# Kernel tuning notes

Hardware: AMD Instinct MI355X
Metric: run time of the kernel (lower is better)

The kernel has to match this reference:

```python
import jax, jax.numpy as jnp
import numpy as np

N, C, H, W = 8, 256, 52, 52
N_WIN, NUM_HEADS, TOPK = 7, 1, 4
RS = (H // N_WIN, W // N_WIN)  # region size (7, 7)
SCALE = C ** -0.5


def _avg_pool_ceil(t):
    # F.avg_pool2d(kernel=RS, stride=RS, ceil_mode=True, count_include_pad=False)
    B, Ch, h_in, w_in = t.shape
    h = -(-h_in // RS[0]); w = -(-w_in // RS[1])
    tp = jnp.pad(t, ((0, 0), (0, 0), (0, h * RS[0] - h_in), (0, w * RS[1] - w_in)))
    s = tp.reshape(B, Ch, h, RS[0], w, RS[1]).sum(axis=(3, 5))
    rc = np.minimum(RS[0], h_in - np.arange(h) * RS[0]).astype(np.float32)
    cc = np.minimum(RS[1], w_in - np.arange(w) * RS[1]).astype(np.float32)
    return s / (rc[:, None] * cc[None, :])


def _nearest_up(t):
    # F.interpolate(mode='nearest', scale_factor=RS) for integer scales == repeat
    return jnp.repeat(jnp.repeat(t, RS[0], axis=2), RS[1], axis=3)


def _grid2seq(t):
    # BCHW -> (B, nhead, nregion, reg_area, head_dim)
    B, Ch, Hp, Wp = t.shape
    rh, rw = Hp // RS[0], Wp // RS[1]
    hd = Ch // NUM_HEADS
    t = t.reshape(B, NUM_HEADS, hd, rh, RS[0], rw, RS[1]).transpose(0, 1, 3, 5, 4, 6, 2)
    return t.reshape(B, NUM_HEADS, rh * rw, RS[0] * RS[1], hd), rh, rw


def _forward(x, y, q_w, q_b, k_w, k_b):
    q = jnp.einsum('nchw,oc->nohw', x, q_w) + q_b[None, :, None, None]
    k = jnp.einsum('nchw,oc->nohw', y, k_w) + k_b[None, :, None, None]
    # routing path uses detached q, k
    q_r = _avg_pool_ceil(jax.lax.stop_gradient(q))  # (B, C, 8, 8)
    k_r = _avg_pool_ceil(jax.lax.stop_gradient(k))
    B, _, h, w = q_r.shape
    nreg = h * w
    a_r = jnp.einsum('nchw,ncyx->nhwyx', q_r, k_r).reshape(B, nreg, nreg)
    idx = jax.lax.top_k(a_r, TOPK)[1]                              # (B, nreg, topk)
    idx = jnp.broadcast_to(idx[:, None], (B, NUM_HEADS, nreg, TOPK))
    a_r = SCALE * a_r
    # coarse scores upsampled over key pixels, then over query pixels
    a1 = _nearest_up(a_r.reshape(B, nreg, h, w))                   # (B, nreg, Hp, Wp)
    Hp, Wp = a1.shape[2], a1.shape[3]
    a1 = _nearest_up(a1.transpose(0, 2, 3, 1).reshape(B, Hp * Wp, h, w))  # (B, Hp*Wp, Hp, Wp)
    reg_area = (Hp * Wp) // nreg
    a6 = a1.reshape(B, NUM_HEADS, nreg, reg_area // NUM_HEADS, nreg, reg_area)
    # fine attention on padded q, k
    pad_b = (RS[0] - H % RS[0]) % RS[0]
    pad_r = (RS[1] - W % RS[1]) % RS[1]
    qp = jnp.pad(q, ((0, 0), (0, 0), (0, pad_b), (0, pad_r)))
    kp = jnp.pad(k, ((0, 0), (0, 0), (0, pad_b), (0, pad_r)))
    q_seq, rh, rw = _grid2seq(qp)   # (B, nh, nreg, reg_area, hd)
    k_seq, _, _ = _grid2seq(kp)
    bI = jnp.arange(B)[:, None, None, None]
    mI = jnp.arange(NUM_HEADS)[None, :, None, None]
    key_g = k_seq[bI, mI, idx]      # gather top-k key regions: (B, nh, nreg, topk, reg_area, hd)
    attn = jnp.einsum('bmrqd,bmrtkd->bmrqtk', q_seq * SCALE, key_g)
    # torch.scatter along dim 4 with index repeated over the t' axis -> duplicate
    # writes to the same slot; serial torch scatter keeps the LAST write (t'=TOPK-1)
    vals = attn[:, :, :, :TOPK, TOPK - 1, :]  # (B, nh, nreg, topk, reg_area)
    rI = jnp.arange(nreg)[None, None, :, None]
    tI = jnp.arange(TOPK)[None, None, None, :]
    corr = a6.at[bI, mI, rI, tI, idx].set(vals)
    # _corr2grid: 10-dim view + 'bmhwpqyxcd->bmhpwqycxd'
    c10 = corr.reshape(B, NUM_HEADS, rh, rw, RS[0], RS[1], rh, rw, RS[0], RS[1])
    c10 = c10.transpose(0, 1, 2, 4, 3, 5, 6, 8, 7, 9)
    Hf, Wf = rh * RS[0], rw * RS[1]
    corr = c10.reshape(B, NUM_HEADS, Hf, Wf, Hf, Wf)
    corr = corr[:, :, :Hf - pad_b, :Wf - pad_r, :Hf - pad_b, :Wf - pad_r]
    return corr.transpose(0, 2, 3, 1, 4, 5)  # (B, H, W, nhead, H, W)


def setup_inputs():
    ks = jax.random.split(jax.random.key(0), 6)
    return {
        'x': jax.random.normal(ks[0], (N, C, H, W), jnp.float32),
        'y': jax.random.normal(ks[1], (N, C, H, W), jnp.float32),
        'q_w': jax.random.normal(ks[2], (C, C), jnp.float32) * (C ** -0.5),
        'q_b': jax.random.normal(ks[3], (C,), jnp.float32) * 0.02,
        'k_w': jax.random.normal(ks[4], (C, C), jnp.float32) * (C ** -0.5),
        'k_b': jax.random.normal(ks[5], (C,), jnp.float32) * 0.02,
    }


def reference(x, y, q_w, q_b, k_w, k_b):
    return _forward(x, y, q_w, q_b, k_w, k_b)
```

## Files before the change

kernel.cpp:

```cpp
#include <hip/hip_runtime.h>

#define NB 8
#define C 256
#define HW 52
#define P (HW*HW)
#define NTOPK 4
#define SCALE 0.0625f

static __device__ __forceinline__ int d7(int v)  { return (v*9363) >> 16; }
static __device__ __forceinline__ int d56(int v) { return (v*18725) >> 20; }
static __device__ __forceinline__ int d13(int v) { return (v*10083) >> 17; }

#define OFF_YR  0
#define OFF_XGT 131072
#define OFF_XRT 655360
#define OFF_M   786432
#define OFF_U   851968
#define OFF_V2  852224
#define OFF_C0  852480
#define OFF_YT  852496

__global__ __launch_bounds__(256) void k1_pool_prep_tr(
    const float* __restrict__ x, const float* __restrict__ y,
    const float* __restrict__ qw, const float* __restrict__ qb,
    const float* __restrict__ kw, const float* __restrict__ kb,
    float* __restrict__ scr)
{
    __shared__ float sm[4*P];
    const int tid = threadIdx.x;
    const int bx = blockIdx.x;

    float* yr  = scr + OFF_YR;
    float* xgT = scr + OFF_XGT;
    float* xrT = scr + OFF_XRT;
    float* M   = scr + OFF_M;
    float* u   = scr + OFF_U;
    float* v2  = scr + OFF_V2;
    float* c0p = scr + OFF_C0;
    float* yT  = scr + OFF_YT;

    if (bx >= 1089) {
        const int tb = bx - 1089;
        const int b = tb / 172;
        const int rem = tb - b*172;
        const int ct = rem / 43;
        const int pt = rem - ct*43;
        const int c0 = ct*64, pos0 = pt*64;
        float* tile = sm;
        const float* ysrc = y + ((size_t)(b*256 + c0))*P;
        #pragma unroll
        for (int p = 0; p < 4; p++) {
            const int cr = p*16 + (tid>>4);
            const int f4 = tid&15;
            const int pos = pos0 + f4*4;
            if (pos < P) {
                const float4 v = *(const float4*)(ysrc + (size_t)cr*P + pos);
                float* d = tile + cr*65 + f4*4;
                d[0]=v.x; d[1]=v.y; d[2]=v.z; d[3]=v.w;
            }
        }
        __syncthreads();
        #pragma unroll
        for (int p = 0; p < 4; p++) {
            const int pj = p*16 + (tid>>4);
            const int c4 = tid&15;
            const int pos = pos0 + pj;
            if (pos < P) {
                float4 v;
                v.x = tile[(c4*4+0)*65 + pj];
                v.y = tile[(c4*4+1)*65 + pj];
                v.z = tile[(c4*4+2)*65 + pj];
                v.w = tile[(c4*4+3)*65 + pj];
                *(float4*)(yT + ((size_t)(b*P + pos))*256 + c0 + c4*4) = v;
            }
        }
        return;
    }

    if (bx >= 1024) {
        const int pb = bx - 1024;
        if (pb == 64) {
            float ua = 0.f, va = 0.f;
            for (int e = 0; e < 256; e++) {
                ua += qb[e] * kw[e*256 + tid];
                va += kb[e] * qw[e*256 + tid];
            }
            u[tid] = ua; v2[tid] = va;
            if (tid == 0) {
                float c = 0.f;
                for (int e = 0; e < 256; e++) c += qb[e]*kb[e];
                c0p[0] = c;
            }
            return;
        }
        const int cx0 = pb * 4;
        float (*wqs)[4] = (float(*)[4])sm;
        *(float4*)&wqs[tid][0] = *(const float4*)(qw + tid*256 + cx0);
        __syncthreads();
        float a0=0.f, a1=0.f, a2=0.f, a3=0.f;
        #pragma unroll 4
        for (int o = 0; o < 256; o++) {
            const float wk = kw[o*256 + tid];
            const float4 wq = *(const float4*)&wqs[o][0];
            a0 += wq.x*wk; a1 += wq.y*wk; a2 += wq.z*wk; a3 += wq.w*wk;
        }
        M[(cx0+0)*256 + tid] = a0;
        M[(cx0+1)*256 + tid] = a1;
        M[(cx0+2)*256 + tid] = a2;
        M[(cx0+3)*256 + tid] = a3;
        return;
    }

    const int w = tid >> 6, lane = tid & 63;
    const int pl = bx*4 + w;
    const int proj = pl >> 11;
    const int bcid = pl & 2047;
    const int bb = bcid >> 8, cc = bcid & 255;
    const float* src = (proj ? y : x) + (size_t)bcid * P;
    float* plane = sm + w*P;
    {
        const float4* s4 = (const float4*)src;
        float4* p4 = (float4*)plane;
        for (int g = lane; g < 676; g += 64) p4[g] = s4[g];
    }
    __syncthreads();
    const int jh = lane >> 3, jw = lane & 7;
    const int y0 = jh*7, x0 = jw*7;
    const int ry = min(7, HW - y0), rx = min(7, HW - x0);
    float s = 0.f;
    for (int dy = 0; dy < ry; ++dy) {
        const float* row = plane + (y0 + dy)*HW + x0;
        for (int dx = 0; dx < rx; ++dx) s += row[dx];
    }
    const float pooled = s / (float)(ry*rx);
    if (proj) {
        yr[bcid*64 + lane] = pooled;
    } else {
        xrT[((size_t)(bb*64) + lane)*256 + cc] = pooled;
        const float* r0 = plane + y0*HW + x0;
        #pragma unroll
        for (int t = 0; t < 4; t++) {
            const float v = (x0 + t < HW) ? r0[t] : 0.f;
            xgT[((size_t)(bb*256) + lane*4 + t)*256 + cc] = v;
        }
    }
}

__global__ __launch_bounds__(256) void k2_topk_vals(
    const float* __restrict__ scr,
    float* __restrict__ arT, int* __restrict__ idxout, float* __restrict__ vals)
{
    const int b = blockIdx.y, r = blockIdx.x;
    const int tid = threadIdx.x, w = tid >> 6, lane = tid & 63;

    const float* yr  = scr + OFF_YR;
    const float* xgT = scr + OFF_XGT;
    const float* xrT = scr + OFF_XRT;
    const float* M   = scr + OFF_M;
    const float* u   = scr + OFF_U;
    const float* v2  = scr + OFF_V2;
    const float* c0p = scr + OFF_C0;
    const float* yT  = scr + OFF_YT;

    __shared__ float Gs[4][256];
    __shared__ float Grs[256];
    __shared__ float pdot[4][64];
    __shared__ float aux[12];
    __shared__ int gsh;
    __shared__ float Ys[49][260];

    const float* xrow0 = xgT + ((size_t)(b*256) + r*4)*256;
    const float* xrow4 = xrT + ((size_t)(b*64) + r)*256;
    {
        float a0=0.f, a1=0.f, a2=0.f, a3=0.f, a4=0.f;
        #pragma unroll 4
        for (int c = 0; c < 256; c++) {
            const float m = M[c*256 + tid];
            a0 += xrow0[c]       * m;
            a1 += xrow0[256 + c] * m;
            a2 += xrow0[512 + c] * m;
            a3 += xrow0[768 + c] * m;
            a4 += xrow4[c]       * m;
        }
        const float uo = u[tid];
        Gs[0][tid] = a0 + uo;
        Gs[1][tid] = a1 + uo;
        Gs[2][tid] = a2 + uo;
        Gs[3][tid] = a3 + uo;
        Grs[tid]   = a4 + uo;
    }
    {
        const float* xh = xrow0 + w*256;
        float hacc = 0.f;
        #pragma unroll
        for (int j = 0; j < 4; j++) {
            const int c = lane + j*64;
            hacc += xh[c] * v2[c];
        }
        #pragma unroll
        for (int off = 32; off >= 1; off >>= 1) hacc += __shfl_xor(hacc, off);
        if (lane == 0) aux[w] = hacc + c0p[0];

        float cacc = xrow4[w*64 + lane] * v2[w*64 + lane];
        #pragma unroll
        for (int off = 32; off >= 1; off >>= 1) cacc += __shfl_xor(cacc, off);
        if (lane == 0) aux[4 + w] = cacc;
    }
    __syncthreads();

    {
        const float* yrB = yr + b*C*64;
        float d = 0.f;
        #pragma unroll 8
        for (int cc = 0; cc < 64; cc++) {
            const int c = w*64 + cc;
            d += Grs[c] * yrB[c*64 + lane];
        }
        pdot[w][lane] = d;
    }
    __syncthreads();

    if (w == 0) {
        const float ci = aux[4] + aux[5] + aux[6] + aux[7] + c0p[0];
        const float dot = pdot[0][lane] + pdot[1][lane] + pdot[2][lane]
                        + pdot[3][lane] + ci;
        arT[(b*64 + lane)*64 + r] = dot * SCALE;
        float v = dot;
        const int my = lane;
        #pragma unroll
        for (int t = 0; t < NTOPK; t++) {
            float bv = v; int bi = my;
            #pragma unroll
            for (int off = 32; off >= 1; off >>= 1) {
                const float ov = __shfl_xor(bv, off);
                const int   oi = __shfl_xor(bi, off);
                if (ov > bv || (ov == bv && oi < bi)) { bv = ov; bi = oi; }
            }
            if (lane == 0) {
                idxout[(b*64 + r)*NTOPK + t] = bi;
                if (t == NTOPK-1) gsh = bi;
            }
            if (my == bi) v = -3.0e38f;
        }
    }
    __syncthreads();

    const int g = gsh;
    const int gy = g >> 3, gx = g & 7;
    for (int i = tid; i < 49*64; i += 256) {
        const int k2 = i >> 6, f4 = i & 63;
        const int dy = d7(k2), dx = k2 - dy*7;
        const int kY = gy*7 + dy, kX = gx*7 + dx;
        float4 v = make_float4(0.f, 0.f, 0.f, 0.f);
        if (kY < HW && kX < HW)
            v = *(const float4*)(yT + ((size_t)(b*P + kY*HW + kX))*256 + f4*4);
        *(float4*)&Ys[k2][f4*4] = v;
    }
    __syncthreads();

    if (tid < NTOPK*49) {
        const int t = tid / 49, k2 = tid - (tid/49)*49;
        const int qX = (r & 7)*7 + t;
        const int dy = d7(k2), dx = k2 - dy*7;
        const int kY = gy*7 + dy, kX = gx*7 + dx;
        float res = 0.f;
        if (qX < HW && kY < HW && kX < HW) {
            const float4* Gp = (const float4*)&Gs[t][0];
            const float4* Yp = (const float4*)&Ys[k2][0];
            float dot = 0.f;
            #pragma unroll 8
            for (int cc = 0; cc < 64; cc++) {
                const float4 a = Gp[cc], yy = Yp[cc];
                dot += a.x*yy.x + a.y*yy.y + a.z*yy.z + a.w*yy.w;
            }
            res = SCALE * (dot + aux[t]);
        }
        vals[((b*64 + r)*NTOPK + t)*49 + k2] = res;
    }
}

__global__ __launch_bounds__(256) void fill_kernel(
    const float* __restrict__ arT, const float* __restrict__ vals,
    const int* __restrict__ idx, float* __restrict__ out)
{
    const int b = blockIdx.y;
    const int yx = blockIdx.x;
    const int Y1 = yx / HW, X1 = yx % HW;
    const int r1 = (Y1/7)*8 + X1/7;
    const int q1 = (Y1%7)*7 + X1%7;
    const int p2 = r1*49 + q1;
    const int yy = p2/56, xx = p2 - 56*yy;
    const int regB = (yy/7)*8 + xx/7;

    __shared__ float acol[64];
    __shared__ float vrow[49];
    const int tid = threadIdx.x;
    if (tid < 64) acol[tid] = arT[(b*64 + regB)*64 + tid];
    int ovr = -1;
    if (q1 < NTOPK) {
        ovr = idx[(b*64 + r1)*NTOPK + q1];
        if (tid < 49) vrow[tid] = vals[((b*64 + r1)*NTOPK + q1)*49 + tid];
    }
    __syncthreads();

    float* plane = out + (size_t)(b*P + yx) * P;
    for (int u = tid; u < 676; u += 256) {
        const int Y2 = d13(u);
        const int g4 = u - Y2*13;
        const int X2b = g4*4;
        const int ry2 = d7(Y2);
        const int my2 = Y2 - ry2*7;
        float res[4];
        #pragma unroll
        for (int j = 0; j < 4; j++) {
            const int X2 = X2b + j;
            const int rx2 = d7(X2);
            const int mx2 = X2 - rx2*7;
            const int r2 = ry2*8 + rx2;
            const int k2 = my2*7 + mx2;
            const int P1 = r2*49 + k2;
            const int Yp = d56(P1);
            const int Xp = P1 - Yp*56;
            const int regA = d7(Yp)*8 + d7(Xp);
            float v = acol[regA];
            if (r2 == ovr) v = vrow[k2];
            res[j] = v;
        }
        float4 o; o.x = res[0]; o.y = res[1]; o.z = res[2]; o.w = res[3];
        *(float4*)(plane + Y2*HW + X2b) = o;
    }
}

extern "C" void kernel_launch(void* const* d_in, const int* in_sizes, int n_in,
                              void* d_out, int out_size, void* d_ws, size_t ws_size,
                              hipStream_t stream)
{
    const float* x  = (const float*)d_in[0];
    const float* y  = (const float*)d_in[1];
    const float* qw = (const float*)d_in[2];
    const float* qb = (const float*)d_in[3];
    const float* kw = (const float*)d_in[4];
    const float* kb = (const float*)d_in[5];
    float* out = (float*)d_out;

    float* scr = out;

    float* ws  = (float*)d_ws;
    float* arT = ws;
    float* vls = arT + 32768;
    int*   idx = (int*)(vls + 100352);

    k1_pool_prep_tr<<<2465, 256, 0, stream>>>(x, y, qw, qb, kw, kb, scr);
    k2_topk_vals<<<dim3(64, 8), 256, 0, stream>>>(scr, arT, idx, vls);
    fill_kernel<<<dim3(P, 8), 256, 0, stream>>>(arT, vls, idx, out);
}
```

Baseline: 116.7 us.

## Split projection GEMM into a tiled shared-memory kernel before top-k

Moves the per-block G = X·M products out of the top-k kernel into a dedicated tiled GEMM kernel with 64x64 shared-memory tiles and 4x4 register blocking. Pooled and gathered x are now stored channel-major with coalesced float4 writes instead of scattered transposed stores. The top-k kernel then just loads the precomputed G rows. The final output fill uses nontemporal stores. This adds a kernel launch and an extra scratch round trip, and the h-term reads in the top-k kernel become strided.

```diff
diff --git a/kernel.cpp b/kernel.cpp
--- a/kernel.cpp
+++ b/kernel.cpp
@@ -7,18 +7,22 @@
 #define NTOPK 4
 #define SCALE 0.0625f
 
+typedef float nt_f32x4 __attribute__((ext_vector_type(4)));
+
 static __device__ __forceinline__ int d7(int v)  { return (v*9363) >> 16; }
 static __device__ __forceinline__ int d56(int v) { return (v*18725) >> 20; }
 static __device__ __forceinline__ int d13(int v) { return (v*10083) >> 17; }
 
-#define OFF_YR  0
-#define OFF_XGT 131072
-#define OFF_XRT 655360
-#define OFF_M   786432
-#define OFF_U   851968
-#define OFF_V2  852224
-#define OFF_C0  852480
-#define OFF_YT  852496
+#define OFF_XR  0
+#define OFF_YR  131072
+#define OFF_XG  262144
+#define OFF_G   786432
+#define OFF_GR  1310720
+#define OFF_M   1441792
+#define OFF_U   1507328
+#define OFF_V2  1507584
+#define OFF_C0  1507840
+#define OFF_YT  1507856
 
 __global__ __launch_bounds__(256) void k1_pool_prep_tr(
     const float* __restrict__ x, const float* __restrict__ y,
@@ -30,9 +34,9 @@
     const int tid = threadIdx.x;
     const int bx = blockIdx.x;
 
+    float* xr  = scr + OFF_XR;
     float* yr  = scr + OFF_YR;
-    float* xgT = scr + OFF_XGT;
-    float* xrT = scr + OFF_XRT;
+    float* xg  = scr + OFF_XG;
     float* M   = scr + OFF_M;
     float* u   = scr + OFF_U;
     float* v2  = scr + OFF_V2;
@@ -115,7 +119,6 @@
     const int pl = bx*4 + w;
     const int proj = pl >> 11;
     const int bcid = pl & 2047;
-    const int bb = bcid >> 8, cc = bcid & 255;
     const float* src = (proj ? y : x) + (size_t)bcid * P;
     float* plane = sm + w*P;
     {
@@ -136,28 +139,92 @@
     if (proj) {
         yr[bcid*64 + lane] = pooled;
     } else {
-        xrT[((size_t)(bb*64) + lane)*256 + cc] = pooled;
+        xr[bcid*64 + lane] = pooled;
         const float* r0 = plane + y0*HW + x0;
-        #pragma unroll
-        for (int t = 0; t < 4; t++) {
-            const float v = (x0 + t < HW) ? r0[t] : 0.f;
-            xgT[((size_t)(bb*256) + lane*4 + t)*256 + cc] = v;
-        }
+        float4 g4;
+        g4.x = r0[0]; g4.y = r0[1]; g4.z = r0[2];
+        g4.w = (x0 + 3 < HW) ? r0[3] : 0.f;
+        *(float4*)&xg[bcid*256 + lane*4] = g4;
     }
 }
 
-__global__ __launch_bounds__(256) void k2_topk_vals(
+__global__ __launch_bounds__(256) void k2_gemms(float* __restrict__ scr)
+{
+    const float* xr = scr + OFF_XR;
+    const float* xg = scr + OFF_XG;
+    float* G  = scr + OFF_G;
+    float* Gr = scr + OFF_GR;
+    const float* M  = scr + OFF_M;
+    const float* uu = scr + OFF_U;
+
+    __shared__ float As[32][64];
+    __shared__ float Bs[32][64];
+    const int tid = threadIdx.x;
+    const int tx = tid & 15, ty = tid >> 4;
+
+    const int un = blockIdx.x;
+    const int b = un / 20;
+    const int rem = un - b*20;
+    const int pt = rem >> 2, ot = rem & 3;
+    const int o0 = ot*64;
+
+    float acc[4][4];
+    #pragma unroll
+    for (int i = 0; i < 4; i++)
+        #pragma unroll
+        for (int j = 0; j < 4; j++) acc[i][j] = 0.f;
+
+    const int lkr = tid >> 3;
+    const int ljc = (tid & 7) * 8;
+    const float* Asrc; int astr;
+    if (pt < 4) { Asrc = xg + (size_t)b*C*256 + pt*64; astr = 256; }
+    else        { Asrc = xr + (size_t)b*C*64;          astr = 64;  }
+
+    for (int k0 = 0; k0 < 256; k0 += 32) {
+        const float4 a0 = *(const float4*)(Asrc + (size_t)(k0 + lkr)*astr + ljc);
+        const float4 a1 = *(const float4*)(Asrc + (size_t)(k0 + lkr)*astr + ljc + 4);
+        const float4 b0 = *(const float4*)(M + (k0 + lkr)*256 + o0 + ljc);
+        const float4 b1 = *(const float4*)(M + (k0 + lkr)*256 + o0 + ljc + 4);
+        __syncthreads();
+        *(float4*)&As[lkr][ljc] = a0; *(float4*)&As[lkr][ljc+4] = a1;
+        *(float4*)&Bs[lkr][ljc] = b0; *(float4*)&Bs[lkr][ljc+4] = b1;
+        __syncthreads();
+        #pragma unroll
+        for (int kk = 0; kk < 32; kk++) {
+            const float4 a = *(const float4*)&As[kk][ty*4];
+            const float4 bb = *(const float4*)&Bs[kk][tx*4];
+            const float av[4] = {a.x, a.y, a.z, a.w};
+            const float bv[4] = {bb.x, bb.y, bb.z, bb.w};
+            #pragma unroll
+            for (int i = 0; i < 4; i++)
+                #pragma unroll
+                for (int j = 0; j < 4; j++) acc[i][j] += av[i]*bv[j];
+        }
+    }
+    const float4 u4 = *(const float4*)(uu + o0 + tx*4);
+    float* base = (pt < 4) ? (G + ((size_t)b*256 + pt*64)*256)
+                           : (Gr + (size_t)b*64*256);
+    #pragma unroll
+    for (int i = 0; i < 4; i++) {
+        float4 ov;
+        ov.x = acc[i][0]+u4.x; ov.y = acc[i][1]+u4.y;
+        ov.z = acc[i][2]+u4.z; ov.w = acc[i][3]+u4.w;
+        *(float4*)(base + (ty*4 + i)*256 + o0 + tx*4) = ov;
+    }
+}
+
+__global__ __launch_bounds__(256) void k3_topk_vals(
     const float* __restrict__ scr,
     float* __restrict__ arT, int* __restrict__ idxout, float* __restrict__ vals)
 {
     const int b = blockIdx.y, r = blockIdx.x;
     const int tid = threadIdx.x, w = tid >> 6, lane = tid & 63;
 
+    const float* xr  = scr + OFF_XR;
     const float* yr  = scr + OFF_YR;
-    const float* xgT = scr + OFF_XGT;
-    const float* xrT = scr + OFF_XRT;
-    const float* M   = scr + OFF_M;
-    const float* u   = scr + OFF_U;
+    const float* xg  = scr + OFF_XG;
+    const float* G   = scr + OFF_G;
+    const float* Gr  = scr + OFF_GR;
     const float* v2  = scr + OFF_V2;
     const float* c0p = scr + OFF_C0;
     const float* yT  = scr + OFF_YT;
@@ -169,39 +236,24 @@
     __shared__ int gsh;
     __shared__ float Ys[49][260];
 
-    const float* xrow0 = xgT + ((size_t)(b*256) + r*4)*256;
-    const float* xrow4 = xrT + ((size_t)(b*64) + r)*256;
+    *(float4*)&Gs[w][lane*4] =
+        *(const float4*)(G + ((size_t)(b*256 + r*4 + w))*256 + lane*4);
+    if (tid < 64)
+        *(float4*)&Grs[tid*4] = *(const float4*)(Gr + ((size_t)(b*64 + r))*256 + tid*4);
     {
-        float a0=0.f, a1=0.f, a2=0.f, a3=0.f, a4=0.f;
-        #pragma unroll 4
-        for (int c = 0; c < 256; c++) {
-            const float m = M[c*256 + tid];
-            a0 += xrow0[c]       * m;
-            a1 += xrow0[256 + c] * m;
-            a2 += xrow0[512 + c] * m;
-            a3 += xrow0[768 + c] * m;
-            a4 += xrow4[c]       * m;
-        }
-        const float uo = u[tid];
-        Gs[0][tid] = a0 + uo;
-        Gs[1][tid] = a1 + uo;
-        Gs[2][tid] = a2 + uo;
-        Gs[3][tid] = a3 + uo;
-        Grs[tid]   = a4 + uo;
-    }
-    {
-        const float* xh = xrow0 + w*256;
+        const int pos = r*4 + w;
         float hacc = 0.f;
         #pragma unroll
         for (int j = 0; j < 4; j++) {
             const int c = lane + j*64;
-            hacc += xh[c] * v2[c];
+            hacc += xg[((size_t)(b*256 + c))*256 + pos] * v2[c];
         }
         #pragma unroll
         for (int off = 32; off >= 1; off >>= 1) hacc += __shfl_xor(hacc, off);
         if (lane == 0) aux[w] = hacc + c0p[0];
 
-        float cacc = xrow4[w*64 + lane] * v2[w*64 + lane];
+        const int c = w*64 + lane;
+        float cacc = xr[(size_t)(b*256 + c)*64 + r] * v2[c];
         #pragma unroll
         for (int off = 32; off >= 1; off >>= 1) cacc += __shfl_xor(cacc, off);
         if (lane == 0) aux[4 + w] = cacc;
@@ -326,8 +378,9 @@
             if (r2 == ovr) v = vrow[k2];
             res[j] = v;
         }
-        float4 o; o.x = res[0]; o.y = res[1]; o.z = res[2]; o.w = res[3];
-        *(float4*)(plane + Y2*HW + X2b) = o;
+        nt_f32x4 o;
+        o.x = res[0]; o.y = res[1]; o.z = res[2]; o.w = res[3];
+        __builtin_nontemporal_store(o, (nt_f32x4*)(plane + Y2*HW + X2b));
     }
 }
 
@@ -351,6 +404,7 @@
     int*   idx = (int*)(vls + 100352);
 
     k1_pool_prep_tr<<<2465, 256, 0, stream>>>(x, y, qw, qb, kw, kb, scr);
-    k2_topk_vals<<<dim3(64, 8), 256, 0, stream>>>(scr, arT, idx, vls);
+    k2_gemms<<<160, 256, 0, stream>>>(scr);
+    k3_topk_vals<<<dim3(64, 8), 256, 0, stream>>>(scr, arT, idx, vls);
     fill_kernel<<<dim3(P, 8), 256, 0, stream>>>(arT, vls, idx, out);
 }
```

New measurement: 106.5 us. 8.7% less time.

## Split projection GEMM into separate wide kernel and coalesce transposed pooled writes

Applied to the files above, without the earlier changes.

Moves the per-region G = x·M projection out of the 512-block topk kernel into a new 640-block kernel that also hosts the y transpose, so the GEMM runs across many more workgroups. The pooling kernel now stages its pooled and gathered values in shared memory and writes them as float4 across four channels, replacing scattered scalar stores. The fill kernel uses nontemporal stores for the large output. This costs an extra launch and an extra round trip of G through global memory.

```diff
diff --git a/kernel.cpp b/kernel.cpp
--- a/kernel.cpp
+++ b/kernel.cpp
@@ -7,6 +7,8 @@
 #define NTOPK 4
 #define SCALE 0.0625f
 
+typedef float nt_f32x4 __attribute__((ext_vector_type(4)));
+
 static __device__ __forceinline__ int d7(int v)  { return (v*9363) >> 16; }
 static __device__ __forceinline__ int d56(int v) { return (v*18725) >> 20; }
 static __device__ __forceinline__ int d13(int v) { return (v*10083) >> 17; }
@@ -14,19 +16,23 @@
 #define OFF_YR  0
 #define OFF_XGT 131072
 #define OFF_XRT 655360
-#define OFF_M   786432
-#define OFF_U   851968
-#define OFF_V2  852224
-#define OFF_C0  852480
-#define OFF_YT  852496
-
-__global__ __launch_bounds__(256) void k1_pool_prep_tr(
+#define OFF_G   786432
+#define OFF_GR  1310720
+#define OFF_M   1441792
+#define OFF_U   1507328
+#define OFF_V2  1507584
+#define OFF_C0  1507840
+#define OFF_YT  1507856
+
+__global__ __launch_bounds__(256) void ka_pool_prep(
     const float* __restrict__ x, const float* __restrict__ y,
     const float* __restrict__ qw, const float* __restrict__ qb,
     const float* __restrict__ kw, const float* __restrict__ kb,
     float* __restrict__ scr)
 {
     __shared__ float sm[4*P];
+    __shared__ float gbuf[4][256];
+    __shared__ float pbuf[4][64];
     const int tid = threadIdx.x;
     const int bx = blockIdx.x;
 
@@ -37,45 +43,6 @@
     float* u   = scr + OFF_U;
     float* v2  = scr + OFF_V2;
     float* c0p = scr + OFF_C0;
-    float* yT  = scr + OFF_YT;
-
-    if (bx >= 1089) {
-        const int tb = bx - 1089;
-        const int b = tb / 172;
-        const int rem = tb - b*172;
-        const int ct = rem / 43;
-        const int pt = rem - ct*43;
-        const int c0 = ct*64, pos0 = pt*64;
-        float* tile = sm;
-        const float* ysrc = y + ((size_t)(b*256 + c0))*P;
-        #pragma unroll
-        for (int p = 0; p < 4; p++) {
-            const int cr = p*16 + (tid>>4);
-            const int f4 = tid&15;
-            const int pos = pos0 + f4*4;
-            if (pos < P) {
-                const float4 v = *(const float4*)(ysrc + (size_t)cr*P + pos);
-                float* d = tile + cr*65 + f4*4;
-                d[0]=v.x; d[1]=v.y; d[2]=v.z; d[3]=v.w;
-            }
-        }
-        __syncthreads();
-        #pragma unroll
-        for (int p = 0; p < 4; p++) {
-            const int pj = p*16 + (tid>>4);
-            const int c4 = tid&15;
-            const int pos = pos0 + pj;
-            if (pos < P) {
-                float4 v;
-                v.x = tile[(c4*4+0)*65 + pj];
-                v.y = tile[(c4*4+1)*65 + pj];
-                v.z = tile[(c4*4+2)*65 + pj];
-                v.w = tile[(c4*4+3)*65 + pj];
-                *(float4*)(yT + ((size_t)(b*P + pos))*256 + c0 + c4*4) = v;
-            }
-        }
-        return;
-    }
 
     if (bx >= 1024) {
         const int pb = bx - 1024;
@@ -115,7 +82,6 @@
     const int pl = bx*4 + w;
     const int proj = pl >> 11;
     const int bcid = pl & 2047;
-    const int bb = bcid >> 8, cc = bcid & 255;
     const float* src = (proj ? y : x) + (size_t)bcid * P;
     float* plane = sm + w*P;
     {
@@ -136,17 +102,115 @@
     if (proj) {
         yr[bcid*64 + lane] = pooled;
     } else {
-        xrT[((size_t)(bb*64) + lane)*256 + cc] = pooled;
+        pbuf[w][lane] = pooled;
         const float* r0 = plane + y0*HW + x0;
-        #pragma unroll
-        for (int t = 0; t < 4; t++) {
-            const float v = (x0 + t < HW) ? r0[t] : 0.f;
-            xgT[((size_t)(bb*256) + lane*4 + t)*256 + cc] = v;
+        gbuf[w][lane*4+0] = r0[0];
+        gbuf[w][lane*4+1] = r0[1];
+        gbuf[w][lane*4+2] = r0[2];
+        gbuf[w][lane*4+3] = (x0 + 3 < HW) ? r0[3] : 0.f;
+        __syncthreads();
+        const int pl0 = bx*4;
+        const int b  = (pl0 & 2047) >> 8;
+        const int c0 = pl0 & 255;
+        {
+            const int pos = tid;
+            float4 v;
+            v.x = gbuf[0][pos]; v.y = gbuf[1][pos];
+            v.z = gbuf[2][pos]; v.w = gbuf[3][pos];
+            *(float4*)(xgT + ((size_t)(b*256 + pos))*256 + c0) = v;
+        }
+        if (tid < 64) {
+            float4 v;
+            v.x = pbuf[0][tid]; v.y = pbuf[1][tid];
+            v.z = pbuf[2][tid]; v.w = pbuf[3][tid];
+            *(float4*)(xrT + ((size_t)(b*64 + tid))*256 + c0) = v;
         }
     }
 }
 
-__global__ __launch_bounds__(256) void k2_topk_vals(
+__global__ __launch_bounds__(256) void kb_gemm_tr(
+    const float* __restrict__ y, float* __restrict__ scr)
+{
+    __shared__ float sm[4160];
+    const int tid = threadIdx.x;
+    const int bx = blockIdx.x;
+
+    const float* xgT = scr + OFF_XGT;
+    const float* xrT = scr + OFF_XRT;
+    const float* M   = scr + OFF_M;
+    const float* uu  = scr + OFF_U;
+    float* G  = scr + OFF_G;
+    float* Gr = scr + OFF_GR;
+    float* yT = scr + OFF_YT;
+
+    if (bx < 640) {
+        const int b = bx / 80;
+        const int pg = bx - b*80;
+        float (*xs)[256] = (float(*)[256])sm;
+        #pragma unroll
+        for (int j = 0; j < 4; j++) {
+            const int R = pg*4 + j;
+            const float* src = (R < 256) ? (xgT + ((size_t)(b*256 + R))*256)
+                                         : (xrT + ((size_t)(b*64 + (R-256)))*256);
+            xs[j][tid] = src[tid];
+        }
+        __syncthreads();
+        float a0=0.f, a1=0.f, a2=0.f, a3=0.f;
+        #pragma unroll 8
+        for (int c = 0; c < 256; c++) {
+            const float m = M[c*256 + tid];
+            a0 += xs[0][c]*m; a1 += xs[1][c]*m;
+            a2 += xs[2][c]*m; a3 += xs[3][c]*m;
+        }
+        const float uo = uu[tid];
+        const float acc[4] = {a0+uo, a1+uo, a2+uo, a3+uo};
+        #pragma unroll
+        for (int j = 0; j < 4; j++) {
+            const int R = pg*4 + j;
+            float* dst = (R < 256) ? (G + ((size_t)(b*256 + R))*256)
+                                   : (Gr + ((size_t)(b*64 + (R-256)))*256);
+            dst[tid] = acc[j];
+        }
+        return;
+    }
+
+    const int tb = bx - 640;
+    const int b = tb / 172;
+    const int rem = tb - b*172;
+    const int ct = rem / 43;
+    const int pt = rem - ct*43;
+    const int c0 = ct*64, pos0 = pt*64;
+    float* tile = sm;
+    const float* ysrc = y + ((size_t)(b*256 + c0))*P;
+    #pragma unroll
+    for (int p = 0; p < 4; p++) {
+        const int cr = p*16 + (tid>>4);
+        const int f4 = tid&15;
+        const int pos = pos0 + f4*4;
+        if (pos < P) {
+            const float4 v = *(const float4*)(ysrc + (size_t)cr*P + pos);
+            float* d = tile + cr*65 + f4*4;
+            d[0]=v.x; d[1]=v.y; d[2]=v.z; d[3]=v.w;
+        }
+    }
+    __syncthreads();
+    #pragma unroll
+    for (int p = 0; p < 4; p++) {
+        const int pj = p*16 + (tid>>4);
+        const int c4 = tid&15;
+        const int pos = pos0 + pj;
+        if (pos < P) {
+            float4 v;
+            v.x = tile[(c4*4+0)*65 + pj];
+            v.y = tile[(c4*4+1)*65 + pj];
+            v.z = tile[(c4*4+2)*65 + pj];
+            v.w = tile[(c4*4+3)*65 + pj];
+            *(float4*)(yT + ((size_t)(b*P + pos))*256 + c0 + c4*4) = v;
+        }
+    }
+}
+
+__global__ __launch_bounds__(256) void kc_topk_vals(
     const float* __restrict__ scr,
     float* __restrict__ arT, int* __restrict__ idxout, float* __restrict__ vals)
 {
@@ -156,8 +220,8 @@
     const float* yr  = scr + OFF_YR;
     const float* xgT = scr + OFF_XGT;
     const float* xrT = scr + OFF_XRT;
-    const float* M   = scr + OFF_M;
-    const float* u   = scr + OFF_U;
+    const float* G   = scr + OFF_G;
+    const float* Gr  = scr + OFF_GR;
     const float* v2  = scr + OFF_V2;
     const float* c0p = scr + OFF_C0;
     const float* yT  = scr + OFF_YT;
@@ -169,39 +233,25 @@
     __shared__ int gsh;
     __shared__ float Ys[49][260];
 
-    const float* xrow0 = xgT + ((size_t)(b*256) + r*4)*256;
-    const float* xrow4 = xrT + ((size_t)(b*64) + r)*256;
+    *(float4*)&Gs[w][lane*4] =
+        *(const float4*)(G + ((size_t)(b*256 + r*4 + w))*256 + lane*4);
+    if (tid < 64)
+        *(float4*)&Grs[tid*4] = *(const float4*)(Gr + ((size_t)(b*64 + r))*256 + tid*4);
     {
-        float a0=0.f, a1=0.f, a2=0.f, a3=0.f, a4=0.f;
-        #pragma unroll 4
-        for (int c = 0; c < 256; c++) {
-            const float m = M[c*256 + tid];
-            a0 += xrow0[c]       * m;
-            a1 += xrow0[256 + c] * m;
-            a2 += xrow0[512 + c] * m;
-            a3 += xrow0[768 + c] * m;
-            a4 += xrow4[c]       * m;
-        }
-        const float uo = u[tid];
-        Gs[0][tid] = a0 + uo;
-        Gs[1][tid] = a1 + uo;
-        Gs[2][tid] = a2 + uo;
-        Gs[3][tid] = a3 + uo;
-        Grs[tid]   = a4 + uo;
-    }
-    {
-        const float* xh = xrow0 + w*256;
+        const float* xrow = xgT + ((size_t)(b*256 + r*4 + w))*256;
         float hacc = 0.f;
         #pragma unroll
         for (int j = 0; j < 4; j++) {
             const int c = lane + j*64;
-            hacc += xh[c] * v2[c];
+            hacc += xrow[c] * v2[c];
         }
         #pragma unroll
         for (int off = 32; off >= 1; off >>= 1) hacc += __shfl_xor(hacc, off);
         if (lane == 0) aux[w] = hacc + c0p[0];
 
-        float cacc = xrow4[w*64 + lane] * v2[w*64 + lane];
+        const float* rrow = xrT + ((size_t)(b*64 + r))*256;
+        const int c = w*64 + lane;
+        float cacc = rrow[c] * v2[c];
         #pragma unroll
         for (int off = 32; off >= 1; off >>= 1) cacc += __shfl_xor(cacc, off);
         if (lane == 0) aux[4 + w] = cacc;
@@ -279,7 +329,7 @@
     }
 }
 
-__global__ __launch_bounds__(256) void fill_kernel(
+__global__ __launch_bounds__(256) void kd_fill(
     const float* __restrict__ arT, const float* __restrict__ vals,
     const int* __restrict__ idx, float* __restrict__ out)
 {
@@ -326,8 +376,9 @@
             if (r2 == ovr) v = vrow[k2];
             res[j] = v;
         }
-        float4 o; o.x = res[0]; o.y = res[1]; o.z = res[2]; o.w = res[3];
-        *(float4*)(plane + Y2*HW + X2b) = o;
+        nt_f32x4 o;
+        o.x = res[0]; o.y = res[1]; o.z = res[2]; o.w = res[3];
+        __builtin_nontemporal_store(o, (nt_f32x4*)(plane + Y2*HW + X2b));
     }
 }
 
@@ -350,7 +401,8 @@
     float* vls = arT + 32768;
     int*   idx = (int*)(vls + 100352);
 
-    k1_pool_prep_tr<<<2465, 256, 0, stream>>>(x, y, qw, qb, kw, kb, scr);
-    k2_topk_vals<<<dim3(64, 8), 256, 0, stream>>>(scr, arT, idx, vls);
-    fill_kernel<<<dim3(P, 8), 256, 0, stream>>>(arT, vls, idx, out);
+    ka_pool_prep<<<1089, 256, 0, stream>>>(x, y, qw, qb, kw, kb, scr);
+    kb_gemm_tr<<<2016, 256, 0, stream>>>(y, scr);
+    kc_topk_vals<<<dim3(64, 8), 256, 0, stream>>>(scr, arT, idx, vls);
+    kd_fill<<<dim3(P, 8), 256, 0, stream>>>(arT, vls, idx, out);
 }
```

After: 108.2 us. 1.08x faster.

## Coalesce transposed scratch writes, stage x rows in LDS, use nontemporal output stores

Applied to the files above, without the earlier changes.

The pooling kernel now gathers the four channel planes of a block into shared buffers and writes the transposed xgT/xrT rows as float4 stores, replacing strided scalar scatters. The routing kernel first loads its five x rows into shared memory and reads them from there in the M-product and dot-product loops, with a higher unroll. The fill kernel writes its large output with nontemporal stores to avoid polluting cache. The change adds a block-wide barrier on the x-projection path and one more shared-memory staging step. Kernels are also renamed.

```diff
diff --git a/kernel.cpp b/kernel.cpp
--- a/kernel.cpp
+++ b/kernel.cpp
@@ -6,6 +6,8 @@
 #define P (HW*HW)
 #define NTOPK 4
 #define SCALE 0.0625f
+
+typedef float nt_f32x4 __attribute__((ext_vector_type(4)));
 
 static __device__ __forceinline__ int d7(int v)  { return (v*9363) >> 16; }
 static __device__ __forceinline__ int d56(int v) { return (v*18725) >> 20; }
@@ -20,13 +22,15 @@
 #define OFF_C0  852480
 #define OFF_YT  852496
 
-__global__ __launch_bounds__(256) void k1_pool_prep_tr(
+__global__ __launch_bounds__(256) void ka_pool_prep_tr(
     const float* __restrict__ x, const float* __restrict__ y,
     const float* __restrict__ qw, const float* __restrict__ qb,
     const float* __restrict__ kw, const float* __restrict__ kb,
     float* __restrict__ scr)
 {
     __shared__ float sm[4*P];
+    __shared__ float gbuf[4][256];
+    __shared__ float pbuf[4][64];
     const int tid = threadIdx.x;
     const int bx = blockIdx.x;
 
@@ -115,7 +119,6 @@
     const int pl = bx*4 + w;
     const int proj = pl >> 11;
     const int bcid = pl & 2047;
-    const int bb = bcid >> 8, cc = bcid & 255;
     const float* src = (proj ? y : x) + (size_t)bcid * P;
     float* plane = sm + w*P;
     {
@@ -136,17 +139,33 @@
     if (proj) {
         yr[bcid*64 + lane] = pooled;
     } else {
-        xrT[((size_t)(bb*64) + lane)*256 + cc] = pooled;
+        pbuf[w][lane] = pooled;
         const float* r0 = plane + y0*HW + x0;
-        #pragma unroll
-        for (int t = 0; t < 4; t++) {
-            const float v = (x0 + t < HW) ? r0[t] : 0.f;
-            xgT[((size_t)(bb*256) + lane*4 + t)*256 + cc] = v;
+        gbuf[w][lane*4+0] = r0[0];
+        gbuf[w][lane*4+1] = r0[1];
+        gbuf[w][lane*4+2] = r0[2];
+        gbuf[w][lane*4+3] = (x0 + 3 < HW) ? r0[3] : 0.f;
+        __syncthreads();
+        const int pl0 = bx*4;
+        const int b  = (pl0 & 2047) >> 8;
+        const int c0 = pl0 & 255;
+        {
+            const int pos = tid;
+            float4 v;
+            v.x = gbuf[0][pos]; v.y = gbuf[1][pos];
+            v.z = gbuf[2][pos]; v.w = gbuf[3][pos];
+            *(float4*)(xgT + ((size_t)(b*256 + pos))*256 + c0) = v;
+        }
+        if (tid < 64) {
+            float4 v;
+            v.x = pbuf[0][tid]; v.y = pbuf[1][tid];
+            v.z = pbuf[2][tid]; v.w = pbuf[3][tid];
+            *(float4*)(xrT + ((size_t)(b*64 + tid))*256 + c0) = v;
         }
     }
 }
 
-__global__ __launch_bounds__(256) void k2_topk_vals(
+__global__ __launch_bounds__(256) void kb_topk_vals(
     const float* __restrict__ scr,
     float* __restrict__ arT, int* __restrict__ idxout, float* __restrict__ vals)
 {
@@ -157,11 +176,12 @@
     const float* xgT = scr + OFF_XGT;
     const float* xrT = scr + OFF_XRT;
     const float* M   = scr + OFF_M;
-    const float* u   = scr + OFF_U;
+    const float* uu  = scr + OFF_U;
     const float* v2  = scr + OFF_V2;
     const float* c0p = scr + OFF_C0;
     const float* yT  = scr + OFF_YT;
 
+    __shared__ float xs[5][256];
     __shared__ float Gs[4][256];
     __shared__ float Grs[256];
     __shared__ float pdot[4][64];
@@ -169,20 +189,22 @@
     __shared__ int gsh;
     __shared__ float Ys[49][260];
 
-    const float* xrow0 = xgT + ((size_t)(b*256) + r*4)*256;
-    const float* xrow4 = xrT + ((size_t)(b*64) + r)*256;
+    #pragma unroll
+    for (int j = 0; j < 4; j++)
+        xs[j][tid] = xgT[((size_t)(b*256 + r*4 + j))*256 + tid];
+    xs[4][tid] = xrT[((size_t)(b*64 + r))*256 + tid];
+    __syncthreads();
+
     {
         float a0=0.f, a1=0.f, a2=0.f, a3=0.f, a4=0.f;
-        #pragma unroll 4
+        #pragma unroll 8
         for (int c = 0; c < 256; c++) {
             const float m = M[c*256 + tid];
-            a0 += xrow0[c]       * m;
-            a1 += xrow0[256 + c] * m;
-            a2 += xrow0[512 + c] * m;
-            a3 += xrow0[768 + c] * m;
-            a4 += xrow4[c]       * m;
-        }
-        const float uo = u[tid];
+            a0 += xs[0][c]*m; a1 += xs[1][c]*m;
+            a2 += xs[2][c]*m; a3 += xs[3][c]*m;
+            a4 += xs[4][c]*m;
+        }
+        const float uo = uu[tid];
         Gs[0][tid] = a0 + uo;
         Gs[1][tid] = a1 + uo;
         Gs[2][tid] = a2 + uo;
@@ -190,18 +212,18 @@
         Grs[tid]   = a4 + uo;
     }
     {
-        const float* xh = xrow0 + w*256;
         float hacc = 0.f;
         #pragma unroll
         for (int j = 0; j < 4; j++) {
             const int c = lane + j*64;
-            hacc += xh[c] * v2[c];
+            hacc += xs[w][c] * v2[c];
         }
         #pragma unroll
         for (int off = 32; off >= 1; off >>= 1) hacc += __shfl_xor(hacc, off);
         if (lane == 0) aux[w] = hacc + c0p[0];
 
-        float cacc = xrow4[w*64 + lane] * v2[w*64 + lane];
+        const int c = w*64 + lane;
+        float cacc = xs[4][c] * v2[c];
         #pragma unroll
         for (int off = 32; off >= 1; off >>= 1) cacc += __shfl_xor(cacc, off);
         if (lane == 0) aux[4 + w] = cacc;
@@ -279,7 +301,7 @@
     }
 }
 
-__global__ __launch_bounds__(256) void fill_kernel(
+__global__ __launch_bounds__(256) void kc_fill(
     const float* __restrict__ arT, const float* __restrict__ vals,
     const int* __restrict__ idx, float* __restrict__ out)
 {
@@ -326,8 +348,9 @@
             if (r2 == ovr) v = vrow[k2];
             res[j] = v;
         }
-        float4 o; o.x = res[0]; o.y = res[1]; o.z = res[2]; o.w = res[3];
-        *(float4*)(plane + Y2*HW + X2b) = o;
+        nt_f32x4 o;
+        o.x = res[0]; o.y = res[1]; o.z = res[2]; o.w = res[3];
+        __builtin_nontemporal_store(o, (nt_f32x4*)(plane + Y2*HW + X2b));
     }
 }
 
@@ -350,7 +373,7 @@
     float* vls = arT + 32768;
     int*   idx = (int*)(vls + 100352);
 
-    k1_pool_prep_tr<<<2465, 256, 0, stream>>>(x, y, qw, qb, kw, kb, scr);
-    k2_topk_vals<<<dim3(64, 8), 256, 0, stream>>>(scr, arT, idx, vls);
-    fill_kernel<<<dim3(P, 8), 256, 0, stream>>>(arT, vls, idx, out);
+    ka_pool_prep_tr<<<2465, 256, 0, stream>>>(x, y, qw, qb, kw, kb, scr);
+    kb_topk_vals<<<dim3(64, 8), 256, 0, stream>>>(scr, arT, idx, vls);
+    kc_fill<<<dim3(P, 8), 256, 0, stream>>>(arT, vls, idx, out);
 }
```

Result: faster. 103.3 us, median of 2 (-11.5%).
